# Kernel optimization log

Hardware: AMD Instinct MI355X
Metric: run time of the kernel (lower is better)

## Reference

```python
import jax, jax.numpy as jnp
import numpy as np

B, N, CIN, COUT, K, L, NNZ = 4, 4096, 128, 128, 10, 50, 65536


def _spmm(idx, vals, X):
    # COO spmm: out[r] += vals * X[c]; idx: [2, nnz], X: [N, F]
    rows, cols = idx[0], idx[1]
    return jax.ops.segment_sum(vals[:, None] * X[cols], rows, num_segments=N)

_bspmm = jax.vmap(_spmm, in_axes=(0, 0, 0))  # batched over leading dim


def _hgnn_layer(phi_idx, phi_val, inv_idx, inv_val, fea, W, d):
    # original: ((phi @ diag(d)) @ phi_inv) @ (fea @ W)
    # identical math, evaluated right-to-left to stay sparse-dense only
    filt = jnp.einsum('bnc,co->bno', fea, W)            # [B,N,COUT]
    y = _bspmm(inv_idx, inv_val, filt)                  # phi_inv @ X
    y = d[None, :, None] * y                            # diag(d) @ .
    return _bspmm(phi_idx, phi_val, y)                  # phi @ .


def setup_inputs() -> dict:
    key = jax.random.key(0)
    ks = jax.random.split(key, 20)

    def coo(ki, kv):
        idx = jax.random.randint(ki, (B, 2, NNZ), 0, N, dtype=jnp.int32)
        val = jax.random.normal(kv, (B, NNZ), jnp.float32) * 0.05
        return idx, val

    phi1_idx, phi1_val = coo(ks[0], ks[1])
    phi1_inv_idx, phi1_inv_val = coo(ks[2], ks[3])
    phi2_idx, phi2_val = coo(ks[4], ks[5])
    phi2_inv_idx, phi2_inv_val = coo(ks[6], ks[7])
    fea = jax.random.normal(ks[8], (B, N, CIN), jnp.float32)
    joblst = jax.random.randint(ks[9], (B, L), 0, N, dtype=jnp.int64)

    xavier = float(np.sqrt(6.0 / (CIN + COUT)))
    W1 = jax.random.uniform(ks[10], (CIN, COUT), jnp.float32, -xavier, xavier)
    W2 = jax.random.uniform(ks[11], (CIN, COUT), jnp.float32, -xavier, xavier)
    d1 = jax.random.uniform(ks[12], (N,), jnp.float32, 0.9, 1.1)
    d2 = jax.random.uniform(ks[13], (N,), jnp.float32, 0.9, 1.1)
    s = float(1.0 / np.sqrt(N))
    W_ih = jax.random.uniform(ks[14], (N, COUT), jnp.float32, -s, s)
    W_hh = jax.random.uniform(ks[15], (N, N), jnp.float32, -s, s)
    b_ih = jax.random.uniform(ks[16], (N,), jnp.float32, -s, s)
    b_hh = jnp.zeros((N,), jnp.float32)
    sd = float(1.0 / np.sqrt(COUT))
    dense_W = jax.random.uniform(ks[17], (K, COUT), jnp.float32, -sd, sd)
    dense_b = jnp.zeros((K,), jnp.float32)
    item_emb = jax.random.normal(ks[18], (N, COUT), jnp.float32) * 0.01

    return dict(phi1_idx=phi1_idx, phi1_val=phi1_val, phi1_inv_idx=phi1_inv_idx,
                phi1_inv_val=phi1_inv_val, phi2_idx=phi2_idx, phi2_val=phi2_val,
                phi2_inv_idx=phi2_inv_idx, phi2_inv_val=phi2_inv_val,
                fea=fea, joblst=joblst, W1=W1, d1=d1, W2=W2, d2=d2,
                W_ih=W_ih, W_hh=W_hh, b_ih=b_ih, b_hh=b_hh,
                dense_W=dense_W, dense_b=dense_b, item_emb=item_emb)


def reference(phi1_idx, phi1_val, phi1_inv_idx, phi1_inv_val,
              phi2_idx, phi2_val, phi2_inv_idx, phi2_inv_val,
              fea, joblst, W1, d1, W2, d2, W_ih, W_hh, b_ih, b_hh,
              dense_W, dense_b, item_emb):
    # two hypergraph conv layers, summed
    out1 = _hgnn_layer(phi1_idx, phi1_val, phi1_inv_idx, phi1_inv_val, fea, W1, d1)
    out2 = _hgnn_layer(phi2_idx, phi2_val, phi2_inv_idx, phi2_inv_val, fea, W2, d2)
    res = out1 + out2                                   # [B,N,COUT]

    # RNN over job history embeddings (all joblst entries valid -> no -1 filter)
    xs = jnp.swapaxes(item_emb[joblst], 0, 1)           # [L,B,COUT]
    h0 = jnp.zeros((fea.shape[0], N), fea.dtype)

    def step(h, x):
        h = jnp.tanh(x @ W_ih.T + h @ W_hh.T + b_ih + b_hh)
        return h, None

    Emb, _ = jax.lax.scan(step, h0, xs)                 # last hidden: [B,N]

    res2 = jax.nn.gelu(jnp.einsum('bno,ko->bnk', res, dense_W) + dense_b,
                       approximate=False)               # [B,N,K]
    # (res3 * Emb2).permute back == res2 * gelu(Emb) broadcast over K
    return jax.nn.sigmoid(res2 * jax.nn.gelu(Emb, approximate=False)[:, :, None])
```

## Files before the change

kernel.cpp:

```cpp
#include <hip/hip_runtime.h>
#include <cstdint>
#include <cstddef>

#define NN   4096
#define LLC  50

__device__ __forceinline__ float bf2f(unsigned short u) {
    return __uint_as_float(((unsigned)u) << 16);
}
__device__ __forceinline__ unsigned short f2bf(float x) {
    unsigned b = __float_as_uint(x);
    return (unsigned short)((b + 0x7fffu + ((b >> 16) & 1u)) >> 16);
}

#if __has_builtin(__builtin_amdgcn_sdot4)
#define SDOT4(a, b, c) __builtin_amdgcn_sdot4((int)(a), (int)(b), (c), false)
#else
__device__ __forceinline__ int sdot4_sw(unsigned a, unsigned b, int c) {
    c += (int)(signed char)(a) * (int)(signed char)(b);
    c += (int)(signed char)(a >> 8) * (int)(signed char)(b >> 8);
    c += (int)(signed char)(a >> 16) * (int)(signed char)(b >> 16);
    c += (int)(signed char)(a >> 24) * (int)(signed char)(b >> 24);
    return c;
}
#define SDOT4(a, b, c) sdot4_sw((a), (b), (c))
#endif

#define DPPADD(v, ctrl, rmask) \
    ((v) + __builtin_amdgcn_update_dpp(0, (v), (ctrl), (rmask), 0xf, true))
__device__ __forceinline__ int wred64(int v) {
    v = DPPADD(v, 0x111, 0xf);
    v = DPPADD(v, 0x112, 0xf);
    v = DPPADD(v, 0x114, 0xf);
    v = DPPADD(v, 0x118, 0xf);
    v = DPPADD(v, 0x142, 0xa);
    v = DPPADD(v, 0x143, 0xc);
    return v;
}

__global__ __launch_bounds__(256) void k_prep(
        const int* __restrict__ i0, const int* __restrict__ i1,
        const int* __restrict__ i2, const int* __restrict__ i3,
        const float* __restrict__ fea,
        const float* __restrict__ W1, const float* __restrict__ W2,
        const float* __restrict__ item_emb, const int* __restrict__ joblst,
        const float* __restrict__ W_ih,
        const float* __restrict__ b_ih, const float* __restrict__ b_hh,
        int* __restrict__ rowptr, int* __restrict__ cursor,
        unsigned short* __restrict__ filt1, unsigned short* __restrict__ filt2,
        float* __restrict__ xp) {
    __shared__ float smem[4096];
    __shared__ int wt4[4];
    int t = threadIdx.x;
    int lane = t & 63, wv = t >> 6;
    int blk = blockIdx.x;

    if (blk < 16) {
        int s = blk;
        int* lc = (int*)smem;
#pragma unroll
        for (int i = 0; i < 16; ++i) lc[t + i * 256] = 0;
        __syncthreads();
        unsigned m = (unsigned)s >> 2, b = (unsigned)s & 3;
        const int* ip = (m == 0) ? i0 : (m == 1) ? i1 : (m == 2) ? i2 : i3;
        const int4* ip4 = (const int4*)(ip + (size_t)b * 131072);
#pragma unroll 4
        for (int i = 0; i < 64; ++i) {
            int4 r4 = ip4[i * 256 + t];
            atomicAdd(&lc[r4.x], 1);
            atomicAdd(&lc[r4.y], 1);
            atomicAdd(&lc[r4.z], 1);
            atomicAdd(&lc[r4.w], 1);
        }
        __syncthreads();
        int loc[16];
        int base = t * 16;
        int run = 0;
#pragma unroll
        for (int i = 0; i < 16; ++i) { loc[i] = run; run += lc[base + i]; }
        int total = run;
        int v = total;
#pragma unroll
        for (int d = 1; d < 64; d <<= 1) { int u = __shfl_up(v, d, 64); if (lane >= d) v += u; }
        if (lane == 63) wt4[wv] = v;
        __syncthreads();
        int pre = v - total;
        for (int i = 0; i < wv; ++i) pre += wt4[i];
        int* rp = rowptr + s * 4097;
        int* cu = cursor + s * 4096;
#pragma unroll
        for (int i = 0; i < 16; ++i) { rp[base + i] = pre + loc[i]; cu[base + i] = pre + loc[i]; }
        if (t == 255) rp[4096] = pre + total;
    } else if (blk < 144) {
        int wx = blk - 16;
        int nb = wx & 15, pb = wx >> 4;
        int p0 = pb * 25;
        for (int idx = t; idx < 25 * 128; idx += 256) {
            int rr = idx >> 7, c = idx & 127;
            int p = p0 + rr;
            int b = p & 3, l = p >> 2;
            int j = joblst[b * LLC + l];
            smem[idx] = item_emb[(size_t)j * 128 + c];
        }
        __syncthreads();
        int n = nb * 256 + t;
        float acc[25];
#pragma unroll
        for (int r = 0; r < 25; ++r) acc[r] = 0.f;
        const float* wn = W_ih + (size_t)n * 128;
        for (int c = 0; c < 128; c += 4) {
            float4 wq = *(const float4*)(wn + c);
#pragma unroll
            for (int r = 0; r < 25; ++r) {
                float4 xr = *(const float4*)&smem[r * 128 + c];
                acc[r] += xr.x * wq.x + xr.y * wq.y + xr.z * wq.z + xr.w * wq.w;
            }
        }
        float bias = b_ih[n] + b_hh[n];
#pragma unroll
        for (int r = 0; r < 25; ++r) xp[(size_t)(p0 + r) * NN + n] = acc[r] + bias;
    } else {
        int rb = (blk - 144) * 32;
#pragma unroll
        for (int i = 0; i < 16; ++i) {
            int idx = t + i * 256;
            smem[idx] = fea[(size_t)rb * 128 + idx];
        }
        __syncthreads();
        int half = t >> 7, tc = t & 127;
        const float* sf = smem + half * 2048;
        float a1[16], a2[16];
#pragma unroll
        for (int r = 0; r < 16; ++r) { a1[r] = 0.f; a2[r] = 0.f; }
        for (int c = 0; c < 128; c += 4) {
            float w10 = W1[(c + 0) * 128 + tc], w11 = W1[(c + 1) * 128 + tc];
            float w12 = W1[(c + 2) * 128 + tc], w13 = W1[(c + 3) * 128 + tc];
            float w20 = W2[(c + 0) * 128 + tc], w21 = W2[(c + 1) * 128 + tc];
            float w22 = W2[(c + 2) * 128 + tc], w23 = W2[(c + 3) * 128 + tc];
#pragma unroll
            for (int r = 0; r < 16; ++r) {
                float4 f = *(const float4*)&sf[r * 128 + c];
                a1[r] += f.x * w10 + f.y * w11 + f.z * w12 + f.w * w13;
                a2[r] += f.x * w20 + f.y * w21 + f.z * w22 + f.w * w23;
            }
        }
#pragma unroll
        for (int r = 0; r < 16; ++r) {
            size_t o = (size_t)(rb + half * 16 + r) * 128 + tc;
            filt1[o] = f2bf(a1[r]);
            filt2[o] = f2bf(a2[r]);
        }
    }
}

__global__ __launch_bounds__(256) void k_scatter(const int* __restrict__ i0, const int* __restrict__ i1,
                                                 const int* __restrict__ i2, const int* __restrict__ i3,
                                                 const float* __restrict__ v0, const float* __restrict__ v1,
                                                 const float* __restrict__ v2, const float* __restrict__ v3,
                                                 const float* __restrict__ d1, const float* __restrict__ d2,
                                                 int* __restrict__ cursor,
                                                 unsigned* __restrict__ ep) {
    unsigned gid = blockIdx.x * 256 + threadIdx.x;
    unsigned s = gid >> 16, e = gid & 65535;
    unsigned m = s >> 2, b = s & 3;
    const int* ip = (m == 0) ? i0 : (m == 1) ? i1 : (m == 2) ? i2 : i3;
    const float* vp = (m == 0) ? v0 : (m == 1) ? v1 : (m == 2) ? v2 : v3;
    int r = ip[(size_t)b * 131072 + e];
    int c = ip[(size_t)b * 131072 + 65536 + e];
    float v = vp[(size_t)b * 65536 + e];
    if (m == 1) v *= d1[c];
    if (m == 3) v *= d2[c];
    int pos = atomicAdd(cursor + s * 4096 + r, 1);
    ep[(size_t)s * 65536 + pos] = ((unsigned)c << 16) | (unsigned)f2bf(v);
}

__device__ __forceinline__ void row_acc(const unsigned* __restrict__ eps, int e0, int e1,
                                        const unsigned* __restrict__ Xd, unsigned bbase,
                                        unsigned lane, float& a0, float& a1) {
    int e = e0;
    for (; e + 8 <= e1; e += 8) {
        unsigned p[8], x[8];
#pragma unroll
        for (int i = 0; i < 8; ++i) p[i] = eps[e + i];
#pragma unroll
        for (int i = 0; i < 8; ++i)
            x[i] = Xd[((size_t)(bbase + (p[i] >> 16)) << 6) + lane];
#pragma unroll
        for (int i = 0; i < 8; ++i) {
            float v = bf2f((unsigned short)p[i]);
            a0 += v * bf2f((unsigned short)x[i]);
            a1 += v * bf2f((unsigned short)(x[i] >> 16));
        }
    }
    for (; e < e1; ++e) {
        unsigned pp = eps[e];
        unsigned xw = Xd[((size_t)(bbase + (pp >> 16)) << 6) + lane];
        float v = bf2f((unsigned short)pp);
        a0 += v * bf2f((unsigned short)xw);
        a1 += v * bf2f((unsigned short)(xw >> 16));
    }
}

__global__ __launch_bounds__(256, 2) void k_mega(
        const float* __restrict__ W_hh,
        const float* __restrict__ xp,
        unsigned* __restrict__ hq,
        int* __restrict__ bar,
        const int* __restrict__ rowptr,
        const unsigned* __restrict__ ep,
        const unsigned short* __restrict__ filt1,
        const unsigned short* __restrict__ filt2,
        unsigned short* __restrict__ y1,
        unsigned short* __restrict__ y2,
        const float* __restrict__ dW,
        const float* __restrict__ db,
        float* __restrict__ g1,
        float* __restrict__ out) {
    __shared__ unsigned hs[4352];
    __shared__ int red[4][16];
    __shared__ unsigned char hpk[4][4][4];
    int t = threadIdx.x;
    int lane = t & 63, wv = t >> 6;
    int blk = blockIdx.x;

    if (blk >= 256) {
        int w = blk - 256;
        int c7 = w & 7;
        {
            unsigned mm = c7 & 1, b = (unsigned)c7 >> 1;
            int s = (mm ? 8 : 0) + (int)b;
            const unsigned* Xd = (const unsigned*)(mm ? filt2 : filt1);
            unsigned* Yd = (unsigned*)(mm ? y2 : y1);
            const int* rp = rowptr + s * 4097;
            const unsigned* eps = ep + (size_t)s * 65536;
            unsigned bbase = b * 4096;
            int g = w >> 3;
            int row0 = (g * 4 + wv) * 16;
            for (int rr = 0; rr < 16; ++rr) {
                int row = row0 + rr;
                float a0 = 0.f, a1 = 0.f;
                row_acc(eps, rp[row], rp[row + 1], Xd, bbase, lane, a0, a1);
                Yd[((size_t)(bbase + row) << 6) + lane] =
                    (unsigned)f2bf(a0) | ((unsigned)f2bf(a1) << 16);
            }
        }
        __syncthreads();
        if (t == 0) {
            __builtin_amdgcn_fence(__ATOMIC_RELEASE, "agent");
            __hip_atomic_fetch_add(&bar[320], 1, __ATOMIC_RELAXED,
                                   __HIP_MEMORY_SCOPE_AGENT);
            while (__hip_atomic_load(&bar[320], __ATOMIC_RELAXED,
                                     __HIP_MEMORY_SCOPE_AGENT) < 512)
                __builtin_amdgcn_s_sleep(4);
            __builtin_amdgcn_fence(__ATOMIC_ACQUIRE, "agent");
        }
        __syncthreads();
        {
            unsigned b = (unsigned)c7 >> 1;
            unsigned bbase = b * 4096;
            const int* rpA = rowptr + (4 + (int)b) * 4097;
            const int* rpB = rowptr + (12 + (int)b) * 4097;
            const unsigned* epA = ep + (size_t)(4 + b) * 65536;
            const unsigned* epB = ep + (size_t)(12 + b) * 65536;
            const unsigned* y1d = (const unsigned*)y1;
            const unsigned* y2d = (const unsigned*)y2;
            int g2 = (w >> 3) * 2 + (w & 1);
            int row0 = (g2 * 4 + wv) * 8;
            float* fs = (float*)hs + wv * 1056;
            for (int rr = 0; rr < 8; ++rr) {
                int row = row0 + rr;
                float a0 = 0.f, a1 = 0.f;
                row_acc(epA, rpA[row], rpA[row + 1], y1d, bbase, lane, a0, a1);
                row_acc(epB, rpB[row], rpB[row + 1], y2d, bbase, lane, a0, a1);
                *(float2*)(fs + rr * 132 + 2 * lane) = make_float2(a0, a1);
            }
#pragma unroll
            for (int pass = 0; pass < 2; ++pass) {
                int task = lane + pass * 64;
                if (task < 80) {
                    int rr = task / 10, k = task - rr * 10;
                    const float* rrp = fs + rr * 132;
                    const float4* wk4 = (const float4*)(dW + (size_t)k * 128);
                    float acc = 0.f;
#pragma unroll
                    for (int c4 = 0; c4 < 32; ++c4) {
                        float4 a = *(const float4*)(rrp + c4 * 4);
                        float4 wq = wk4[c4];
                        acc += a.x * wq.x + a.y * wq.y + a.z * wq.z + a.w * wq.w;
                    }
                    float pre = acc + db[k];
                    float gg = 0.5f * pre * (1.f + erff(pre * 0.70710678118f));
                    g1[(size_t)(bbase + row0 + rr) * 10 + k] = gg;
                }
            }
        }
        __syncthreads();
        if (t == 0) {
            __builtin_amdgcn_fence(__ATOMIC_RELEASE, "agent");
            __hip_atomic_fetch_add(&bar[352], 1, __ATOMIC_RELAXED,
                                   __HIP_MEMORY_SCOPE_AGENT);
        }
        return;
    }

    int row_base = ((blk & 7) * 32 + (blk >> 3)) * 16;
    int wrow = row_base + wv * 4;

    uint4 W[4][4];
    {
        const float* wsrc = W_hh + (size_t)wrow * 4096;
#pragma unroll
        for (int r = 0; r < 4; ++r)
#pragma unroll
            for (int k4 = 0; k4 < 4; ++k4) {
                unsigned q[4];
#pragma unroll
                for (int i = 0; i < 4; ++i) {
                    const float* p = wsrc + (size_t)r * 4096 + (lane * 16 + k4 * 4 + i) * 4;
                    float4 w = *(const float4*)p;
                    int q0 = (int)rintf(fminf(fmaxf(w.x * 8192.f, -127.f), 127.f));
                    int q1 = (int)rintf(fminf(fmaxf(w.y * 8192.f, -127.f), 127.f));
                    int q2 = (int)rintf(fminf(fmaxf(w.z * 8192.f, -127.f), 127.f));
                    int q3 = (int)rintf(fminf(fmaxf(w.w * 8192.f, -127.f), 127.f));
                    q[i] = (q0 & 0xff) | ((q1 & 0xff) << 8) | ((q2 & 0xff) << 16) | ((q3 & 0xff) << 24);
                }
                W[r][k4] = make_uint4(q[0], q[1], q[2], q[3]);
            }
    }

    const float SC = 1.f / (8192.f * 127.f);

    for (int l = 0; l < LLC; ++l) {
        if (l > 0) {
            const unsigned* src = hq + (size_t)((l - 1) & 1) * 4096;
            unsigned sval[16];
#pragma unroll
            for (int k = 0; k < 16; ++k)
                sval[k] = __hip_atomic_load(src + t + k * 256, __ATOMIC_RELAXED,
                                            __HIP_MEMORY_SCOPE_AGENT);
#pragma unroll
            for (int k = 0; k < 16; ++k) hs[t + k * 256] = sval[k];
            __syncthreads();

            __builtin_amdgcn_s_setprio(1);
            uint4 H[4][4];
#pragma unroll
            for (int b = 0; b < 4; ++b)
#pragma unroll
                for (int k4 = 0; k4 < 4; ++k4)
                    H[b][k4] = ((const uint4*)hs)[k4 * 256 + b * 64 + lane];
            int acc[4][4];
#pragma unroll
            for (int r = 0; r < 4; ++r)
#pragma unroll
                for (int b = 0; b < 4; ++b) acc[r][b] = 0;
#pragma unroll
            for (int k4 = 0; k4 < 4; ++k4)
#pragma unroll
                for (int r = 0; r < 4; ++r)
#pragma unroll
                    for (int b = 0; b < 4; ++b) {
                        acc[r][b] = SDOT4(W[r][k4].x, H[b][k4].x, acc[r][b]);
                        acc[r][b] = SDOT4(W[r][k4].y, H[b][k4].y, acc[r][b]);
                        acc[r][b] = SDOT4(W[r][k4].z, H[b][k4].z, acc[r][b]);
                        acc[r][b] = SDOT4(W[r][k4].w, H[b][k4].w, acc[r][b]);
                    }
#pragma unroll
            for (int r = 0; r < 4; ++r)
#pragma unroll
                for (int b = 0; b < 4; ++b) acc[r][b] = wred64(acc[r][b]);
            if (lane == 63) {
#pragma unroll
                for (int b = 0; b < 4; ++b) {
                    int4 q = { acc[0][b], acc[1][b], acc[2][b], acc[3][b] };
                    *(int4*)&red[wv][b * 4] = q;
                }
            }
            __builtin_amdgcn_s_setprio(0);
        }
        float hnew = 0.f;
        if (lane < 16) {
            int b = lane >> 2, rr = lane & 3;
            int row = wrow + rr;
            float a = (l > 0) ? (float)red[wv][lane] * SC : 0.f;
            float pre = a + xp[(size_t)(l * 4 + b) * NN + row];
            hnew = tanhf(pre);
            int q = (int)rintf(hnew * 127.f);
            hpk[wv][b][rr] = (unsigned char)(q & 0xff);
        }
        if (l < LLC - 1) {
            if (lane < 4) {
                int b = lane;
                unsigned d = *(const unsigned*)&hpk[wv][b][0];
                int hk = (row_base >> 2) + wv;
                int phys = ((hk >> 2) & 3) * 1024 + b * 256 + (hk >> 4) * 4 + (hk & 3);
                __hip_atomic_store(hq + (size_t)(l & 1) * 4096 + phys, d,
                                   __ATOMIC_RELAXED, __HIP_MEMORY_SCOPE_AGENT);
            }
            __syncthreads();
            if (t == 0) {
                int g = blk & 7;
                int old = __hip_atomic_fetch_add(&bar[g * 32], 1, __ATOMIC_RELAXED,
                                                 __HIP_MEMORY_SCOPE_AGENT);
                if ((old & 31) == 31)
                    __hip_atomic_fetch_add(&bar[256], 1, __ATOMIC_RELAXED,
                                           __HIP_MEMORY_SCOPE_AGENT);
                int target = 8 * (l + 1);
                while (__hip_atomic_load(&bar[256], __ATOMIC_RELAXED,
                                         __HIP_MEMORY_SCOPE_AGENT) < target)
                    __builtin_amdgcn_s_sleep(2);
            }
            __syncthreads();
        } else {
            if (t == 0) {
                while (__hip_atomic_load(&bar[352], __ATOMIC_RELAXED,
                                         __HIP_MEMORY_SCOPE_AGENT) < 512)
                    __builtin_amdgcn_s_sleep(2);
            }
            __syncthreads();
            if (lane < 16) {
                int b = lane >> 2, rr = lane & 3;
                int row = wrow + rr;
                float ge = 0.5f * hnew * (1.f + erff(hnew * 0.70710678118f));
                size_t gb = ((size_t)b * NN + row) * 10;
#pragma unroll
                for (int k = 0; k < 10; ++k) {
                    float gv = __hip_atomic_load(g1 + gb + k, __ATOMIC_RELAXED,
                                                 __HIP_MEMORY_SCOPE_AGENT);
                    out[gb + k] = 1.f / (1.f + __expf(-gv * ge));
                }
            }
        }
    }
}

extern "C" void kernel_launch(void* const* d_in, const int* in_sizes, int n_in,
                              void* d_out, int out_size, void* d_ws, size_t ws_size,
                              hipStream_t stream) {
    const int*   phi1_idx = (const int*)d_in[0];
    const float* phi1_val = (const float*)d_in[1];
    const int*   inv1_idx = (const int*)d_in[2];
    const float* inv1_val = (const float*)d_in[3];
    const int*   phi2_idx = (const int*)d_in[4];
    const float* phi2_val = (const float*)d_in[5];
    const int*   inv2_idx = (const int*)d_in[6];
    const float* inv2_val = (const float*)d_in[7];
    const float* fea      = (const float*)d_in[8];
    const int*   joblst   = (const int*)d_in[9];
    const float* W1       = (const float*)d_in[10];
    const float* d1       = (const float*)d_in[11];
    const float* W2       = (const float*)d_in[12];
    const float* d2       = (const float*)d_in[13];
    const float* W_ih     = (const float*)d_in[14];
    const float* W_hh     = (const float*)d_in[15];
    const float* b_ih     = (const float*)d_in[16];
    const float* b_hh     = (const float*)d_in[17];
    const float* dense_W  = (const float*)d_in[18];
    const float* dense_b  = (const float*)d_in[19];
    const float* item_emb = (const float*)d_in[20];

    float* ws = (float*)d_ws;
    unsigned short* filt1 = (unsigned short*)ws;
    unsigned short* filt2 = (unsigned short*)(ws + 1048576);
    unsigned short* y1    = (unsigned short*)(ws + 2097152);
    unsigned short* y2    = (unsigned short*)(ws + 3145728);
    float* g1   = ws + 4194304;
    float* xp   = ws + 6291456;
    unsigned* hq  = (unsigned*)(ws + 7127040);
    int*   rowptr = (int*)(ws + 11395072);
    int*   cursor = (int*)(ws + 11460624);
    unsigned* ep  = (unsigned*)(ws + 11526160);
    int*   bar    = (int*)(ws + 12574736);

    hipMemsetAsync(bar, 0, 2048, stream);

    k_prep<<<656, 256, 0, stream>>>(inv1_idx, phi1_idx, inv2_idx, phi2_idx,
                                    fea, W1, W2, item_emb, joblst,
                                    W_ih, b_ih, b_hh,
                                    rowptr, cursor, filt1, filt2, xp);

    k_scatter<<<4096, 256, 0, stream>>>(inv1_idx, phi1_idx, inv2_idx, phi2_idx,
                                        inv1_val, phi1_val, inv2_val, phi2_val,
                                        d1, d2, cursor, ep);

    k_mega<<<768, 256, 0, stream>>>(W_hh, xp, hq, bar,
                                    rowptr, ep, filt1, filt2, y1, y2,
                                    dense_W, dense_b, g1, (float*)d_out);
}
```

Baseline: 502.4 us.

## Fold COO scatter into prep histogram blocks using LDS cursors

Removes the separate k_scatter kernel and the barrier memset. Each of the 16 histogram blocks in k_prep now scatters its own sparse matrix's edges into CSR order, using LDS atomics on a shared cursor array instead of global atomics. The barrier buffer is zeroed inside k_prep instead of by hipMemsetAsync. This saves two launches and the global atomic traffic, but the scatter for 16 matrices of 65536 edges now runs on only 16 blocks, which may lengthen the critical path of k_prep.

```diff
diff --git a/kernel.cpp b/kernel.cpp
--- a/kernel.cpp
+++ b/kernel.cpp
@@ -41,14 +41,17 @@
 __global__ __launch_bounds__(256) void k_prep(
         const int* __restrict__ i0, const int* __restrict__ i1,
         const int* __restrict__ i2, const int* __restrict__ i3,
+        const float* __restrict__ v0, const float* __restrict__ v1,
+        const float* __restrict__ v2, const float* __restrict__ v3,
+        const float* __restrict__ dd1, const float* __restrict__ dd2,
         const float* __restrict__ fea,
         const float* __restrict__ W1, const float* __restrict__ W2,
         const float* __restrict__ item_emb, const int* __restrict__ joblst,
         const float* __restrict__ W_ih,
         const float* __restrict__ b_ih, const float* __restrict__ b_hh,
-        int* __restrict__ rowptr, int* __restrict__ cursor,
+        int* __restrict__ rowptr, unsigned* __restrict__ ep,
         unsigned short* __restrict__ filt1, unsigned short* __restrict__ filt2,
-        float* __restrict__ xp) {
+        float* __restrict__ xp, int* __restrict__ bar) {
     __shared__ float smem[4096];
     __shared__ int wt4[4];
     int t = threadIdx.x;
@@ -58,15 +61,19 @@
     if (blk < 16) {
         int s = blk;
         int* lc = (int*)smem;
+        if (blk == 0) { bar[t] = 0; bar[t + 256] = 0; }
 #pragma unroll
         for (int i = 0; i < 16; ++i) lc[t + i * 256] = 0;
         __syncthreads();
         unsigned m = (unsigned)s >> 2, b = (unsigned)s & 3;
         const int* ip = (m == 0) ? i0 : (m == 1) ? i1 : (m == 2) ? i2 : i3;
-        const int4* ip4 = (const int4*)(ip + (size_t)b * 131072);
+        const float* vp = (m == 0) ? v0 : (m == 1) ? v1 : (m == 2) ? v2 : v3;
+        const int4* r4p = (const int4*)(ip + (size_t)b * 131072);
+        const int4* c4p = (const int4*)(ip + (size_t)b * 131072 + 65536);
+        const float4* v4p = (const float4*)(vp + (size_t)b * 65536);
 #pragma unroll 4
         for (int i = 0; i < 64; ++i) {
-            int4 r4 = ip4[i * 256 + t];
+            int4 r4 = r4p[i * 256 + t];
             atomicAdd(&lc[r4.x], 1);
             atomicAdd(&lc[r4.y], 1);
             atomicAdd(&lc[r4.z], 1);
@@ -87,10 +94,32 @@
         int pre = v - total;
         for (int i = 0; i < wv; ++i) pre += wt4[i];
         int* rp = rowptr + s * 4097;
-        int* cu = cursor + s * 4096;
-#pragma unroll
-        for (int i = 0; i < 16; ++i) { rp[base + i] = pre + loc[i]; cu[base + i] = pre + loc[i]; }
+#pragma unroll
+        for (int i = 0; i < 16; ++i) {
+            int off = pre + loc[i];
+            rp[base + i] = off;
+            lc[base + i] = off;
+        }
         if (t == 255) rp[4096] = pre + total;
+        __syncthreads();
+        unsigned* eps = ep + (size_t)s * 65536;
+#define SCAT1(RR, CC, VV) {                                                    \
+            float vvv = (VV);                                                  \
+            if (m == 1) vvv *= dd1[CC];                                        \
+            if (m == 3) vvv *= dd2[CC];                                        \
+            int pos = atomicAdd(&lc[RR], 1);                                   \
+            eps[pos] = ((unsigned)(CC) << 16) | (unsigned)f2bf(vvv); }
+#pragma unroll 4
+        for (int i = 0; i < 64; ++i) {
+            int4 r4 = r4p[i * 256 + t];
+            int4 c4 = c4p[i * 256 + t];
+            float4 vv = v4p[i * 256 + t];
+            SCAT1(r4.x, c4.x, vv.x)
+            SCAT1(r4.y, c4.y, vv.y)
+            SCAT1(r4.z, c4.z, vv.z)
+            SCAT1(r4.w, c4.w, vv.w)
+        }
+#undef SCAT1
     } else if (blk < 144) {
         int wx = blk - 16;
         int nb = wx & 15, pb = wx >> 4;
@@ -151,27 +180,6 @@
             filt2[o] = f2bf(a2[r]);
         }
     }
-}
-
-__global__ __launch_bounds__(256) void k_scatter(const int* __restrict__ i0, const int* __restrict__ i1,
-                                                 const int* __restrict__ i2, const int* __restrict__ i3,
-                                                 const float* __restrict__ v0, const float* __restrict__ v1,
-                                                 const float* __restrict__ v2, const float* __restrict__ v3,
-                                                 const float* __restrict__ d1, const float* __restrict__ d2,
-                                                 int* __restrict__ cursor,
-                                                 unsigned* __restrict__ ep) {
-    unsigned gid = blockIdx.x * 256 + threadIdx.x;
-    unsigned s = gid >> 16, e = gid & 65535;
-    unsigned m = s >> 2, b = s & 3;
-    const int* ip = (m == 0) ? i0 : (m == 1) ? i1 : (m == 2) ? i2 : i3;
-    const float* vp = (m == 0) ? v0 : (m == 1) ? v1 : (m == 2) ? v2 : v3;
-    int r = ip[(size_t)b * 131072 + e];
-    int c = ip[(size_t)b * 131072 + 65536 + e];
-    float v = vp[(size_t)b * 65536 + e];
-    if (m == 1) v *= d1[c];
-    if (m == 3) v *= d2[c];
-    int pos = atomicAdd(cursor + s * 4096 + r, 1);
-    ep[(size_t)s * 65536 + pos] = ((unsigned)c << 16) | (unsigned)f2bf(v);
 }
 
 __device__ __forceinline__ void row_acc(const unsigned* __restrict__ eps, int e0, int e1,
@@ -468,20 +476,14 @@
     float* xp   = ws + 6291456;
     unsigned* hq  = (unsigned*)(ws + 7127040);
     int*   rowptr = (int*)(ws + 11395072);
-    int*   cursor = (int*)(ws + 11460624);
     unsigned* ep  = (unsigned*)(ws + 11526160);
     int*   bar    = (int*)(ws + 12574736);
 
-    hipMemsetAsync(bar, 0, 2048, stream);
-
     k_prep<<<656, 256, 0, stream>>>(inv1_idx, phi1_idx, inv2_idx, phi2_idx,
-                                    fea, W1, W2, item_emb, joblst,
+                                    inv1_val, phi1_val, inv2_val, phi2_val,
+                                    d1, d2, fea, W1, W2, item_emb, joblst,
                                     W_ih, b_ih, b_hh,
-                                    rowptr, cursor, filt1, filt2, xp);
-
-    k_scatter<<<4096, 256, 0, stream>>>(inv1_idx, phi1_idx, inv2_idx, phi2_idx,
-                                        inv1_val, phi1_val, inv2_val, phi2_val,
-                                        d1, d2, cursor, ep);
+                                    rowptr, ep, filt1, filt2, xp, bar);
 
     k_mega<<<768, 256, 0, stream>>>(W_hh, xp, hq, bar,
                                     rowptr, ep, filt1, filt2, y1, y2,
```

Result: slower. 560.5 us (+11.6%).
